# Performance work log

Hardware: AMD Instinct MI355X
Metric: run time of the kernel (lower is better)

Reference implementation:

```python
import jax, jax.numpy as jnp
import numpy as np

K = 10
ALPHA = 0.1


def setup_inputs() -> dict:
    key = jax.random.key(0)
    k1, k2, k3, k4 = jax.random.split(key, 4)
    N, E, D_IN, D_OUT = 100000, 3200000, 128, 64
    x = jax.random.normal(k1, (N, D_IN), dtype=jnp.float32)
    edge_index = jax.random.randint(k2, (2, E), 0, N, dtype=jnp.int64)
    W = jax.random.normal(k3, (D_IN, D_OUT), dtype=jnp.float32) / np.sqrt(D_IN)
    b = jax.random.normal(k4, (D_OUT,), dtype=jnp.float32) * 0.01
    return {"x": x, "edge_index": edge_index, "W": W, "b": b}


def reference(x, edge_index, W, b):
    N = x.shape[0]
    # gcn_norm with self-loops (PyG default for APPNP when edge_weight is None)
    loop = jnp.arange(N, dtype=edge_index.dtype)
    src = jnp.concatenate([edge_index[0], loop])  # [E+N]
    dst = jnp.concatenate([edge_index[1], loop])
    ew = jnp.ones(src.shape[0], dtype=x.dtype)
    deg = jax.ops.segment_sum(ew, dst, num_segments=N)  # in-degree incl. self-loop
    dinv = jnp.where(deg > 0, jax.lax.rsqrt(deg), 0.0)
    norm = dinv[src] * ew * dinv[dst]  # [E+N]

    # K-step personalized PageRank propagation: h = (1-alpha) * A_hat h + alpha * x
    h = x
    for _ in range(K):
        msg = h[src] * norm[:, None]  # gather + scale, [E+N, D]
        agg = jax.ops.segment_sum(msg, dst, num_segments=N)  # scatter-add
        h = (1.0 - ALPHA) * agg + ALPHA * x

    return h @ W + b
```

## Files before the change

### kernel.cpp

```cpp
#include <hip/hip_runtime.h>
#include <hip/hip_fp16.h>
#include <math.h>


#define BSH 8

typedef _Float16 h2_t __attribute__((ext_vector_type(2)));


__global__ void zero_i32(int* __restrict__ p, int n) {
    int i = blockIdx.x * blockDim.x + threadIdx.x;
    if (i < n) p[i] = 0;
}

__global__ void zero_dummy(__half2* __restrict__ b0, __half2* __restrict__ b1,
                           __half2* __restrict__ b2, int N) {
    int t = threadIdx.x;
    if (t >= 96) return;
    __half2* b = (t < 32) ? b0 : (t < 64) ? b1 : b2;
    b[(size_t)N * 32 + (t & 31)] = __floats2half2_rn(0.f, 0.f);
}


__global__ void __launch_bounds__(256) bucket_hist_k(const int* __restrict__ dst, int E,
                                                     int* __restrict__ bktcnt) {
    __shared__ int hist[400];
    int t = threadIdx.x;
    for (int i = t; i < 400; i += 256) hist[i] = 0;
    __syncthreads();
    int e0 = blockIdx.x * 4096 + t;
#pragma unroll
    for (int i = 0; i < 16; ++i) {
        int e = e0 + i * 256;
        if (e < E) atomicAdd(&hist[dst[e] >> BSH], 1);
    }
    __syncthreads();
    for (int b = t; b < 400; b += 256) {
        int c = hist[b];
        if (c > 0) atomicAdd(&bktcnt[b], c);
    }
}


__global__ void bucket_scan_k(const int* __restrict__ bktcnt, int nb, int E,
                              int* __restrict__ bktbase, int* __restrict__ bktcur) {
    __shared__ int s[256];
    int t = threadIdx.x;
    int C = (nb + 255) / 256;
    int b0 = t * C;
    int loc[8]; int sum = 0;
    for (int i = 0; i < C; ++i) {
        int v = (b0 + i < nb) ? bktcnt[b0 + i] : 0;
        loc[i] = sum; sum += v;
    }
    s[t] = sum; __syncthreads();
    for (int off = 1; off < 256; off <<= 1) {
        int v = (t >= off) ? s[t - off] : 0;
        __syncthreads();
        s[t] += v;
        __syncthreads();
    }
    int excl = s[t] - sum;
    for (int i = 0; i < C; ++i)
        if (b0 + i < nb) {
            int e0 = excl + loc[i];
            bktbase[b0 + i] = e0;
            bktcur[(b0 + i) * 16] = e0;
        }
    if (t == 0) bktbase[nb] = E;
}


__global__ void __launch_bounds__(256) binsort_k(const int* __restrict__ src,
                                                 const int* __restrict__ dst, int E,
                                                 int* __restrict__ bktcur,
                                                 unsigned* __restrict__ binned) {
    __shared__ int hist[400], gbase[400], lcur[400];
    int t = threadIdx.x;
    for (int i = t; i < 400; i += 256) { hist[i] = 0; lcur[i] = 0; }
    __syncthreads();

    int e0 = blockIdx.x * 4096 + t;
    unsigned rec[16]; int bk[16];
#pragma unroll
    for (int i = 0; i < 16; ++i) {
        int e = e0 + i * 256;
        if (e < E) {
            int s = src[e], d = dst[e];
            bk[i]  = d >> BSH;
            rec[i] = ((unsigned)s << BSH) | (unsigned)(d & 255);
            atomicAdd(&hist[bk[i]], 1);
        } else bk[i] = -1;
    }
    __syncthreads();
    for (int b = t; b < 400; b += 256) {
        int c = hist[b];
        if (c > 0) gbase[b] = atomicAdd(&bktcur[b * 16], c);
    }
    __syncthreads();
#pragma unroll
    for (int i = 0; i < 16; ++i) {
        if (bk[i] >= 0) {
            int loc = atomicAdd(&lcur[bk[i]], 1);
            binned[gbase[bk[i]] + loc] = rec[i];
        }
    }
}


__global__ void __launch_bounds__(256) fill2_k(const unsigned* __restrict__ binned,
                                               const int* __restrict__ bktbase,
                                               int N, int E, int NB,
                                               int* __restrict__ rowptr,
                                               float* __restrict__ dinv,
                                               int* __restrict__ col) {
    __shared__ int cnt[256], excl[256], lcur[256];
    int b = blockIdx.x, t = threadIdx.x;
    int beg = bktbase[b], end = bktbase[b + 1];
    cnt[t] = 0;
    __syncthreads();
    for (int i = beg + t; i < end; i += 256)
        atomicAdd(&cnt[binned[i] & 255u], 1);
    __syncthreads();
    int v = cnt[t];
    excl[t] = v;
    __syncthreads();
    for (int off = 1; off < 256; off <<= 1) {
        int u = (t >= off) ? excl[t - off] : 0;
        __syncthreads();
        excl[t] += u;
        __syncthreads();
    }
    int ex = excl[t] - v;
    lcur[t] = ex;
    int d = (b << BSH) + t;
    if (d < N) {
        rowptr[d] = beg + ex;
        dinv[d] = rsqrtf((float)(v + 1));
    }
    if (b == NB - 1 && t == 0) rowptr[N] = E;
    __syncthreads();
    for (int i = beg + t; i < end; i += 256) {
        unsigned r = binned[i];
        int loc = atomicAdd(&lcur[r & 255u], 1);
        col[beg + loc] = (int)(r >> BSH);
    }
}


__global__ void __launch_bounds__(256) gemm_k(const float* __restrict__ x,
                                              const float* __restrict__ W,
                                              const float* __restrict__ dinv,
                                              __half2* __restrict__ g0f,
                                              __half2* __restrict__ g0h, int N) {
    __shared__ float xs[64 * 133];
    int t = threadIdx.x;
    int n0 = blockIdx.x * 64;
    for (int f = t; f < 64 * 32; f += 256) {
        int r = f >> 5, c4 = f & 31;
        int n = n0 + r;
        float4 v = (n < N) ? ((const float4*)x)[(size_t)n * 32 + c4]
                           : make_float4(0.f, 0.f, 0.f, 0.f);
        float* dp = &xs[r * 133 + c4 * 4];
        dp[0] = v.x; dp[1] = v.y; dp[2] = v.z; dp[3] = v.w;
    }
    __syncthreads();
    int tr = t & 15, tc = t >> 4;
    int j0 = tr * 4, r0 = tc * 4;
    const float4* W4 = (const float4*)W;
    float acc[4][4] = {};
#pragma unroll 8
    for (int k = 0; k < 128; ++k) {
        float4 wv = W4[k * 16 + tr];
#pragma unroll
        for (int i = 0; i < 4; ++i) {
            float xv = xs[(r0 + i) * 133 + k];
            acc[i][0] += xv * wv.x; acc[i][1] += xv * wv.y;
            acc[i][2] += xv * wv.z; acc[i][3] += xv * wv.w;
        }
    }
    int h0 = j0 >> 1;
#pragma unroll
    for (int i = 0; i < 4; ++i) {
        int n = n0 + r0 + i;
        if (n < N) {
            float dn = dinv[n];
            __half2* gf = &g0f[(size_t)n * 32 + h0];
            gf[0] = __floats2half2_rn(acc[i][0], acc[i][1]);
            gf[1] = __floats2half2_rn(acc[i][2], acc[i][3]);
            __half2* gp = &g0h[(size_t)n * 32 + h0];
            gp[0] = __floats2half2_rn(acc[i][0] * dn, acc[i][1] * dn);
            gp[1] = __floats2half2_rn(acc[i][2] * dn, acc[i][3] * dn);
        }
    }
}


__global__ void __launch_bounds__(256) prop_k(const __half2* __restrict__ gin,
                                              const __half2* __restrict__ g0f,
                                              __half2* __restrict__ gout,
                                              float* __restrict__ outf,
                                              const int* __restrict__ rowptr,
                                              const int* __restrict__ cols,
                                              const float* __restrict__ dinv,
                                              const float* __restrict__ bias,
                                              int N, int final_step) {
    int gw = (blockIdx.x * blockDim.x + threadIdx.x) >> 6;
    int lane = threadIdx.x & 63;
    if (gw >= N) return;
    int sub = lane >> 3;
    int q   = lane & 7;
    int l32 = lane & 31;

    int beg = rowptr[gw], end = rowptr[gw + 1];
    int deg = end - beg;

    const char* gb = (const char*)gin;

    float di    = dinv[gw];
    float4 giv  = *(const float4*)(gb + (size_t)gw * 128 + q * 16);
    float4 g0v4 = *(const float4*)((const char*)g0f + (size_t)gw * 128 + q * 16);

    const h2_t SEL_LO = {(_Float16)1.f, (_Float16)0.f};
    const h2_t SEL_HI = {(_Float16)0.f, (_Float16)1.f};

    float a[8] = {};

    int full = deg & ~31;
    for (int base = 0; base < full; base += 32) {
        int ci = cols[beg + base + l32];
#pragma unroll
        for (int i = 0; i < 4; ++i) {
            int c = __shfl(ci, i * 8 + sub, 64);
            float4 v = *(const float4*)(gb + (size_t)c * 128 + q * 16);
            union { float4 f; h2_t h[4]; } uv; uv.f = v;
#pragma unroll
            for (int u = 0; u < 4; ++u) {
                a[2 * u]     = __builtin_amdgcn_fdot2(uv.h[u], SEL_LO, a[2 * u],     false);
                a[2 * u + 1] = __builtin_amdgcn_fdot2(uv.h[u], SEL_HI, a[2 * u + 1], false);
            }
        }
    }
    int m = deg - full;
    if (m > 0) {
        int ci = cols[beg + full + (l32 < m ? l32 : 0)];
#pragma unroll 4
        for (int i = 0; i * 8 < m; ++i) {
            int e = i * 8 + sub;
            int c = __shfl(ci, e, 64);
            if (e >= m) c = N;
            float4 v = *(const float4*)(gb + (size_t)c * 128 + q * 16);
            union { float4 f; h2_t h[4]; } uv; uv.f = v;
#pragma unroll
            for (int u = 0; u < 4; ++u) {
                a[2 * u]     = __builtin_amdgcn_fdot2(uv.h[u], SEL_LO, a[2 * u],     false);
                a[2 * u + 1] = __builtin_amdgcn_fdot2(uv.h[u], SEL_HI, a[2 * u + 1], false);
            }
        }
    }

#pragma unroll
    for (int off = 8; off < 64; off <<= 1) {
#pragma unroll
        for (int u = 0; u < 8; ++u) a[u] += __shfl_xor(a[u], off, 64);
    }

    if (sub == 0) {
        const __half2* gih  = (const __half2*)&giv;
        const __half2* g0h2 = (const __half2*)&g0v4;
        float r[8];
#pragma unroll
        for (int u = 0; u < 4; ++u) {
            float2 gi = __half22float2(gih[u]);
            float2 g0 = __half22float2(g0h2[u]);
            r[2 * u]     = 0.9f * di * (a[2 * u]     + gi.x) + 0.1f * g0.x;
            r[2 * u + 1] = 0.9f * di * (a[2 * u + 1] + gi.y) + 0.1f * g0.y;
        }
        if (final_step) {
            float4 b0 = ((const float4*)bias)[2 * q];
            float4 b1 = ((const float4*)bias)[2 * q + 1];
            float4 o0 = make_float4(r[0] + b0.x, r[1] + b0.y, r[2] + b0.z, r[3] + b0.w);
            float4 o1 = make_float4(r[4] + b1.x, r[5] + b1.y, r[6] + b1.z, r[7] + b1.w);
            float4* op = (float4*)(outf + (size_t)gw * 64 + q * 8);
            op[0] = o0; op[1] = o1;
        } else {
            __half2 o[4];
#pragma unroll
            for (int u = 0; u < 4; ++u)
                o[u] = __floats2half2_rn(di * r[2 * u], di * r[2 * u + 1]);
            *(float4*)((char*)gout + (size_t)gw * 128 + q * 16) = *(float4*)o;
        }
    }
}


extern "C" void kernel_launch(void* const* d_in, const int* in_sizes, int n_in,
                              void* d_out, int out_size, void* d_ws, size_t ws_size,
                              hipStream_t stream) {
    const float* x  = (const float*)d_in[0];
    const int*   ei = (const int*)d_in[1];
    const float* W  = (const float*)d_in[2];
    const float* b  = (const float*)d_in[3];
    float* out = (float*)d_out;

    const int N = in_sizes[0] / 128;
    const int E = in_sizes[1] / 2;
    const int* src = ei;
    const int* dst = ei + E;
    const int NB = (N + 255) >> BSH;

    char* w = (char*)d_ws;
    size_t off = 0;
    auto alloc = [&](size_t bytes) -> void* {
        void* p = w + off;
        off += (bytes + 255) & ~(size_t)255;
        return p;
    };
    const size_t fp16buf = (size_t)(N + 1) * 32 * sizeof(__half2);
    __half2*  g0h    = (__half2*) alloc(fp16buf);
    __half2*  bufA   = (__half2*) alloc(fp16buf);
    __half2*  bufB   = (__half2*) alloc(fp16buf);
    __half2*  g0f    = (__half2*) alloc(fp16buf);
    int*      cols   = (int*)     alloc((size_t)E * 4);
    unsigned* binned = (unsigned*)alloc((size_t)E * 4);
    int*      rowptr = (int*)     alloc((size_t)(N + 1) * 4);
    int*      bktcnt = (int*)     alloc((size_t)NB * 4);
    int*      bktbase= (int*)     alloc((size_t)(NB + 1) * 4);
    int*      bktcur = (int*)     alloc((size_t)NB * 16 * 4);
    float*    dinvv  = (float*)   alloc((size_t)N * 4);

    const int nblkB = (E + 4095) / 4096;

    zero_i32<<<(NB + 255) / 256, 256, 0, stream>>>(bktcnt, NB);
    bucket_hist_k<<<nblkB, 256, 0, stream>>>(dst, E, bktcnt);
    zero_dummy<<<1, 96, 0, stream>>>(g0h, bufA, bufB, N);
    bucket_scan_k<<<1, 256, 0, stream>>>(bktcnt, NB, E, bktbase, bktcur);
    binsort_k<<<nblkB, 256, 0, stream>>>(src, dst, E, bktcur, binned);
    fill2_k<<<NB, 256, 0, stream>>>(binned, bktbase, N, E, NB, rowptr, dinvv, cols);

    gemm_k<<<(N + 63) / 64, 256, 0, stream>>>(x, W, dinvv, g0f, g0h, N);

    const int nblkP = (N * 64 + 255) / 256;
    const __half2* gin = g0h;
    __half2* pp[2] = {bufA, bufB};
    for (int k = 0; k < 10; ++k) {
        const bool fin = (k == 9);
        __half2* gout = pp[k & 1];
        prop_k<<<nblkP, 256, 0, stream>>>(gin, g0f, gout, out, rowptr, cols,
                                          dinvv, b, N, fin ? 1 : 0);
        gin = gout;
    }
}
```

Measured before the change: 753.4 us.

## Split feature buffers into four column slices mapped to XCD pairs for L2 locality

Stores the 64-wide fp16 feature matrix as four 16-column slices, each laid out contiguously. Each propagation block is assigned to one slice by block-ID modulo 8, so that, assuming round-robin block dispatch across the eight XCDs, each pair of XCDs gathers only one slice of about 3.2 MB that can stay resident in its L2. The cost is four times as many wave-rows per step, narrower 8-byte gathers and more cols/rowptr reads, and the benefit rests on an undocumented dispatch order. It also leaves dead code that computes an unused U8 output.

Result: slower. 1.452 ms (+92.7%).

```diff
diff --git a/kernel.cpp b/kernel.cpp
--- a/kernel.cpp
+++ b/kernel.cpp
@@ -4,8 +4,10 @@
 
 
 #define BSH 8
+#define NSL 4
 
 typedef _Float16 h2_t __attribute__((ext_vector_type(2)));
+union U8 { uint2 u; h2_t h[2]; };
 
 
 __global__ void zero_i32(int* __restrict__ p, int n) {
@@ -18,7 +20,9 @@
     int t = threadIdx.x;
     if (t >= 96) return;
     __half2* b = (t < 32) ? b0 : (t < 64) ? b1 : b2;
-    b[(size_t)N * 32 + (t & 31)] = __floats2half2_rn(0.f, 0.f);
+    int r = t & 31;
+    int s = r >> 3, h = r & 7;
+    b[((size_t)s * (N + 1) + N) * 8 + h] = __floats2half2_rn(0.f, 0.f);
 }
 
 
@@ -151,7 +155,7 @@
 __global__ void __launch_bounds__(256) gemm_k(const float* __restrict__ x,
                                               const float* __restrict__ W,
                                               const float* __restrict__ dinv,
-                                              __half2* __restrict__ g0f,
+                                              __half2* __restrict__ g0t,
                                               __half2* __restrict__ g0h, int N) {
     __shared__ float xs[64 * 133];
     int t = threadIdx.x;
@@ -166,7 +170,7 @@
     }
     __syncthreads();
     int tr = t & 15, tc = t >> 4;
-    int j0 = tr * 4, r0 = tc * 4;
+    int r0 = tc * 4;
     const float4* W4 = (const float4*)W;
     float acc[4][4] = {};
 #pragma unroll 8
@@ -179,116 +183,117 @@
             acc[i][2] += xv * wv.z; acc[i][3] += xv * wv.w;
         }
     }
-    int h0 = j0 >> 1;
+    int slice = tr >> 2;
+    int o = (tr & 3) * 2;
 #pragma unroll
     for (int i = 0; i < 4; ++i) {
         int n = n0 + r0 + i;
         if (n < N) {
             float dn = dinv[n];
-            __half2* gf = &g0f[(size_t)n * 32 + h0];
-            gf[0] = __floats2half2_rn(acc[i][0], acc[i][1]);
-            gf[1] = __floats2half2_rn(acc[i][2], acc[i][3]);
-            __half2* gp = &g0h[(size_t)n * 32 + h0];
-            gp[0] = __floats2half2_rn(acc[i][0] * dn, acc[i][1] * dn);
-            gp[1] = __floats2half2_rn(acc[i][2] * dn, acc[i][3] * dn);
+            size_t rb = ((size_t)slice * (N + 1) + n) * 8;
+            g0t[rb + o]     = __floats2half2_rn(acc[i][0], acc[i][1]);
+            g0t[rb + o + 1] = __floats2half2_rn(acc[i][2], acc[i][3]);
+            g0h[rb + o]     = __floats2half2_rn(acc[i][0] * dn, acc[i][1] * dn);
+            g0h[rb + o + 1] = __floats2half2_rn(acc[i][2] * dn, acc[i][3] * dn);
         }
     }
 }
 
 
 __global__ void __launch_bounds__(256) prop_k(const __half2* __restrict__ gin,
-                                              const __half2* __restrict__ g0f,
+                                              const __half2* __restrict__ g0t,
                                               __half2* __restrict__ gout,
                                               float* __restrict__ outf,
                                               const int* __restrict__ rowptr,
                                               const int* __restrict__ cols,
                                               const float* __restrict__ dinv,
                                               const float* __restrict__ bias,
-                                              int N, int final_step) {
-    int gw = (blockIdx.x * blockDim.x + threadIdx.x) >> 6;
+                                              int N, int nseq, int final_step) {
+    int bid = blockIdx.x;
+    int xcd = bid & 7;
+    int slice = xcd >> 1;
+    int seq = (bid >> 3) * 2 + (xcd & 1);
+    if (seq >= nseq) return;
+    int gw = seq * 4 + (threadIdx.x >> 6);
+    if (gw >= N) return;
+
     int lane = threadIdx.x & 63;
-    if (gw >= N) return;
-    int sub = lane >> 3;
-    int q   = lane & 7;
+    int sub = lane >> 2;
+    int q   = lane & 3;
     int l32 = lane & 31;
+    int qo  = q * 8;
+
+    size_t srow = (size_t)slice * (N + 1);
+    const char* gb = (const char*)gin + srow * 32;
 
     int beg = rowptr[gw], end = rowptr[gw + 1];
     int deg = end - beg;
-
-    const char* gb = (const char*)gin;
-
-    float di    = dinv[gw];
-    float4 giv  = *(const float4*)(gb + (size_t)gw * 128 + q * 16);
-    float4 g0v4 = *(const float4*)((const char*)g0f + (size_t)gw * 128 + q * 16);
+    float di = dinv[gw];
+
+    U8 gi; gi.u = *(const uint2*)(gb + (size_t)gw * 32 + qo);
+    U8 g0; g0.u = *(const uint2*)((const char*)g0t + (srow + gw) * 32 + qo);
 
     const h2_t SEL_LO = {(_Float16)1.f, (_Float16)0.f};
     const h2_t SEL_HI = {(_Float16)0.f, (_Float16)1.f};
 
-    float a[8] = {};
+    float a[4] = {};
 
     int full = deg & ~31;
     for (int base = 0; base < full; base += 32) {
         int ci = cols[beg + base + l32];
 #pragma unroll
-        for (int i = 0; i < 4; ++i) {
-            int c = __shfl(ci, i * 8 + sub, 64);
-            float4 v = *(const float4*)(gb + (size_t)c * 128 + q * 16);
-            union { float4 f; h2_t h[4]; } uv; uv.f = v;
-#pragma unroll
-            for (int u = 0; u < 4; ++u) {
-                a[2 * u]     = __builtin_amdgcn_fdot2(uv.h[u], SEL_LO, a[2 * u],     false);
-                a[2 * u + 1] = __builtin_amdgcn_fdot2(uv.h[u], SEL_HI, a[2 * u + 1], false);
-            }
+        for (int i = 0; i < 2; ++i) {
+            int c = __shfl(ci, i * 16 + sub, 64);
+            U8 v; v.u = *(const uint2*)(gb + (size_t)c * 32 + qo);
+            a[0] = __builtin_amdgcn_fdot2(v.h[0], SEL_LO, a[0], false);
+            a[1] = __builtin_amdgcn_fdot2(v.h[0], SEL_HI, a[1], false);
+            a[2] = __builtin_amdgcn_fdot2(v.h[1], SEL_LO, a[2], false);
+            a[3] = __builtin_amdgcn_fdot2(v.h[1], SEL_HI, a[3], false);
         }
     }
     int m = deg - full;
     if (m > 0) {
         int ci = cols[beg + full + (l32 < m ? l32 : 0)];
-#pragma unroll 4
-        for (int i = 0; i * 8 < m; ++i) {
-            int e = i * 8 + sub;
+#pragma unroll 2
+        for (int i = 0; i * 16 < m; ++i) {
+            int e = i * 16 + sub;
             int c = __shfl(ci, e, 64);
             if (e >= m) c = N;
-            float4 v = *(const float4*)(gb + (size_t)c * 128 + q * 16);
-            union { float4 f; h2_t h[4]; } uv; uv.f = v;
-#pragma unroll
-            for (int u = 0; u < 4; ++u) {
-                a[2 * u]     = __builtin_amdgcn_fdot2(uv.h[u], SEL_LO, a[2 * u],     false);
-                a[2 * u + 1] = __builtin_amdgcn_fdot2(uv.h[u], SEL_HI, a[2 * u + 1], false);
-            }
-        }
-    }
-
-#pragma unroll
-    for (int off = 8; off < 64; off <<= 1) {
-#pragma unroll
-        for (int u = 0; u < 8; ++u) a[u] += __shfl_xor(a[u], off, 64);
+            U8 v; v.u = *(const uint2*)(gb + (size_t)c * 32 + qo);
+            a[0] = __builtin_amdgcn_fdot2(v.h[0], SEL_LO, a[0], false);
+            a[1] = __builtin_amdgcn_fdot2(v.h[0], SEL_HI, a[1], false);
+            a[2] = __builtin_amdgcn_fdot2(v.h[1], SEL_LO, a[2], false);
+            a[3] = __builtin_amdgcn_fdot2(v.h[1], SEL_HI, a[3], false);
+        }
+    }
+
+#pragma unroll
+    for (int off = 4; off < 64; off <<= 1) {
+#pragma unroll
+        for (int u = 0; u < 4; ++u) a[u] += __shfl_xor(a[u], off, 64);
     }
 
     if (sub == 0) {
-        const __half2* gih  = (const __half2*)&giv;
-        const __half2* g0h2 = (const __half2*)&g0v4;
-        float r[8];
-#pragma unroll
-        for (int u = 0; u < 4; ++u) {
-            float2 gi = __half22float2(gih[u]);
-            float2 g0 = __half22float2(g0h2[u]);
-            r[2 * u]     = 0.9f * di * (a[2 * u]     + gi.x) + 0.1f * g0.x;
-            r[2 * u + 1] = 0.9f * di * (a[2 * u + 1] + gi.y) + 0.1f * g0.y;
-        }
+        float2 gi0 = __half22float2(*(__half2*)&gi.h[0]);
+        float2 gi1 = __half22float2(*(__half2*)&gi.h[1]);
+        float2 g00 = __half22float2(*(__half2*)&g0.h[0]);
+        float2 g01 = __half22float2(*(__half2*)&g0.h[1]);
+        float r0 = 0.9f * di * (a[0] + gi0.x) + 0.1f * g00.x;
+        float r1 = 0.9f * di * (a[1] + gi0.y) + 0.1f * g00.y;
+        float r2 = 0.9f * di * (a[2] + gi1.x) + 0.1f * g01.x;
+        float r3 = 0.9f * di * (a[3] + gi1.y) + 0.1f * g01.y;
         if (final_step) {
-            float4 b0 = ((const float4*)bias)[2 * q];
-            float4 b1 = ((const float4*)bias)[2 * q + 1];
-            float4 o0 = make_float4(r[0] + b0.x, r[1] + b0.y, r[2] + b0.z, r[3] + b0.w);
-            float4 o1 = make_float4(r[4] + b1.x, r[5] + b1.y, r[6] + b1.z, r[7] + b1.w);
-            float4* op = (float4*)(outf + (size_t)gw * 64 + q * 8);
-            op[0] = o0; op[1] = o1;
+            float4 bv = ((const float4*)bias)[slice * 4 + q];
+            float4* op = (float4*)(outf + (size_t)gw * 64 + slice * 16 + q * 4);
+            *op = make_float4(r0 + bv.x, r1 + bv.y, r2 + bv.z, r3 + bv.w);
         } else {
-            __half2 o[4];
-#pragma unroll
-            for (int u = 0; u < 4; ++u)
-                o[u] = __floats2half2_rn(di * r[2 * u], di * r[2 * u + 1]);
-            *(float4*)((char*)gout + (size_t)gw * 128 + q * 16) = *(float4*)o;
+            U8 o;
+            o.h[0] = (h2_t)__floats2half2_rn(di * r0, di * r1).data;
+            o.h[1] = (h2_t)__floats2half2_rn(di * r2, di * r3).data;
+            __half2 o0 = __floats2half2_rn(di * r0, di * r1);
+            __half2 o1 = __floats2half2_rn(di * r2, di * r3);
+            __half2* gp = (__half2*)((char*)gout + (srow + gw) * 32 + qo);
+            gp[0] = o0; gp[1] = o1;
         }
     }
 }
@@ -316,11 +321,11 @@
         off += (bytes + 255) & ~(size_t)255;
         return p;
     };
-    const size_t fp16buf = (size_t)(N + 1) * 32 * sizeof(__half2);
+    const size_t fp16buf = (size_t)NSL * (N + 1) * 32;
     __half2*  g0h    = (__half2*) alloc(fp16buf);
     __half2*  bufA   = (__half2*) alloc(fp16buf);
     __half2*  bufB   = (__half2*) alloc(fp16buf);
-    __half2*  g0f    = (__half2*) alloc(fp16buf);
+    __half2*  g0t    = (__half2*) alloc(fp16buf);
     int*      cols   = (int*)     alloc((size_t)E * 4);
     unsigned* binned = (unsigned*)alloc((size_t)E * 4);
     int*      rowptr = (int*)     alloc((size_t)(N + 1) * 4);
@@ -338,16 +343,18 @@
     binsort_k<<<nblkB, 256, 0, stream>>>(src, dst, E, bktcur, binned);
     fill2_k<<<NB, 256, 0, stream>>>(binned, bktbase, N, E, NB, rowptr, dinvv, cols);
 
-    gemm_k<<<(N + 63) / 64, 256, 0, stream>>>(x, W, dinvv, g0f, g0h, N);
-
-    const int nblkP = (N * 64 + 255) / 256;
+    gemm_k<<<(N + 63) / 64, 256, 0, stream>>>(x, W, dinvv, g0t, g0h, N);
+
+    const int nseq  = (N + 3) / 4;
+    const int pairs = (nseq + 1) / 2;
+    const int grid  = pairs * 8;
     const __half2* gin = g0h;
     __half2* pp[2] = {bufA, bufB};
     for (int k = 0; k < 10; ++k) {
         const bool fin = (k == 9);
         __half2* gout = pp[k & 1];
-        prop_k<<<nblkP, 256, 0, stream>>>(gin, g0f, gout, out, rowptr, cols,
-                                          dinvv, b, N, fin ? 1 : 0);
+        prop_k<<<grid, 256, 0, stream>>>(gin, g0t, gout, out, rowptr, cols,
+                                         dinvv, b, N, nseq, fin ? 1 : 0);
         gin = gout;
     }
 }
```
